# Performance work log

Hardware: AMD Instinct MI355X
Metric: run time of the kernel (lower is better)

Reference implementation:

```python
import jax, jax.numpy as jnp
import numpy as np
import math

HEAD_DIM = 128
N_HEADS = 32
N_KV_HEADS = 8
HIDDEN = 4096
ROPE_BASE = 10000.0


def _rope_cos_sin(position_ids):
    # inv_freq: [D/2]
    inv_freq = 1.0 / (ROPE_BASE ** (jnp.arange(0, HEAD_DIM, 2, dtype=jnp.float32) / HEAD_DIM))
    freqs = position_ids.astype(jnp.float32)[..., None] * inv_freq  # [B,S,D/2]
    emb = jnp.concatenate([freqs, freqs], axis=-1)  # [B,S,D]
    return jnp.cos(emb), jnp.sin(emb)


def _rotate_half(x):
    x1, x2 = jnp.split(x, 2, axis=-1)
    return jnp.concatenate([-x2, x1], axis=-1)


def setup_inputs() -> dict:
    key = jax.random.key(0)
    ks = jax.random.split(key, 5)
    B, S = 1, 2048
    inp = {
        "hidden_states": jax.random.normal(ks[0], (B, S, HIDDEN), dtype=jnp.float32),
        "position_ids": jnp.arange(B * S, dtype=jnp.int32).reshape(B, S),
        "Wq": jax.random.normal(ks[1], (HIDDEN, N_HEADS * HEAD_DIM), dtype=jnp.float32) * 0.02,
        "Wk": jax.random.normal(ks[2], (HIDDEN, N_KV_HEADS * HEAD_DIM), dtype=jnp.float32) * 0.02,
        "Wv": jax.random.normal(ks[3], (HIDDEN, N_KV_HEADS * HEAD_DIM), dtype=jnp.float32) * 0.02,
        "Wo": jax.random.normal(ks[4], (N_HEADS * HEAD_DIM, HIDDEN), dtype=jnp.float32) * 0.02,
    }
    return inp


def reference(hidden_states, position_ids, Wq, Wk, Wv, Wo):
    B, S, _ = hidden_states.shape
    G = N_HEADS // N_KV_HEADS

    q = (hidden_states @ Wq).reshape(B, S, N_HEADS, HEAD_DIM).transpose(0, 2, 1, 3)      # [B,H,S,D]
    k = (hidden_states @ Wk).reshape(B, S, N_KV_HEADS, HEAD_DIM).transpose(0, 2, 1, 3)   # [B,Hkv,S,D]
    v = (hidden_states @ Wv).reshape(B, S, N_KV_HEADS, HEAD_DIM).transpose(0, 2, 1, 3)

    cos, sin = _rope_cos_sin(position_ids)          # [B,S,D]
    cos = cos[:, None, :, :]                         # [B,1,S,D]
    sin = sin[:, None, :, :]
    q = q * cos + _rotate_half(q) * sin
    k = k * cos + _rotate_half(k) * sin

    # GQA head expansion (repeat_interleave over head dim)
    k = jnp.repeat(k, G, axis=1)                     # [B,H,S,D]
    v = jnp.repeat(v, G, axis=1)

    scale = 1.0 / math.sqrt(HEAD_DIM)
    scores = jnp.einsum("bhqd,bhkd->bhqk", q, k) * scale  # [B,H,S,S]
    causal = jnp.triu(jnp.full((S, S), -jnp.inf, dtype=scores.dtype), k=1)
    scores = scores + causal[None, None]
    probs = jax.nn.softmax(scores.astype(jnp.float32), axis=-1).astype(q.dtype)
    ctx = jnp.einsum("bhqk,bhkd->bhqd", probs, v)    # [B,H,S,D]
    ctx = ctx.transpose(0, 2, 1, 3).reshape(B, S, N_HEADS * HEAD_DIM)
    return ctx @ Wo
```

## Files before the change

### kernel.cpp

```cpp
#include <hip/hip_runtime.h>
#include <hip/hip_bf16.h>
#include <math.h>

#define SEQ 2048
#define NHEADS 32
#define NKVH 8
#define HD 128
#define HIDDEN 4096

typedef unsigned short u16;
typedef unsigned int u32;
typedef __attribute__((ext_vector_type(8))) __bf16 bf16x8;
typedef __attribute__((ext_vector_type(4))) float f32x4;
typedef __attribute__((ext_vector_type(4))) u16 u16x4;
typedef __attribute__((ext_vector_type(4))) u32 u32x4;

__device__ __forceinline__ u16 f2bf(float f) {
  u32 u = __builtin_bit_cast(u32, f);
  u32 r = (u + 0x7fffu + ((u >> 16) & 1u)) >> 16;
  return (u16)r;
}
__device__ __forceinline__ float bf2f(u16 h) {
  return __builtin_bit_cast(float, ((u32)h) << 16);
}
__device__ __forceinline__ void gload_lds16(const void* g, void* l) {
  __builtin_amdgcn_global_load_lds(
      (const __attribute__((address_space(1))) u32*)g,
      (__attribute__((address_space(3))) u32*)l, 16, 0, 0);
}

__global__ void __launch_bounds__(256) conv_f2b_vec(const float* __restrict__ in,
                                                    u16* __restrict__ out, const int n) {
  const int i = (blockIdx.x * 256 + threadIdx.x) * 4;
  if (i >= n) return;
  const float4 v = *(const float4*)(in + i);
  u16x4 o;
  o.x = f2bf(v.x); o.y = f2bf(v.y); o.z = f2bf(v.z); o.w = f2bf(v.w);
  *(u16x4*)(out + i) = o;
}

__global__ void __launch_bounds__(256) trans_f2b(const float* __restrict__ in,
                                                 u16* __restrict__ out, const int R, const int C) {
  __shared__ float tile[32][33];
  const int c0 = blockIdx.x * 32, r0 = blockIdx.y * 32;
  const int tx = threadIdx.x & 31, ty = threadIdx.x >> 5;
#pragma unroll
  for (int i = 0; i < 4; ++i)
    tile[ty + i * 8][tx] = in[(size_t)(r0 + ty + i * 8) * C + c0 + tx];
  __syncthreads();
#pragma unroll
  for (int i = 0; i < 4; ++i)
    out[(size_t)(c0 + ty + i * 8) * R + r0 + tx] = f2bf(tile[tx][ty + i * 8]);
}

__global__ void __launch_bounds__(256) trans_b2b(const u16* __restrict__ in,
                                                 u16* __restrict__ out, const int R, const int C) {
  __shared__ u16 tile[32][34];
  const int c0 = blockIdx.x * 32, r0 = blockIdx.y * 32;
  const int tx = threadIdx.x & 31, ty = threadIdx.x >> 5;
#pragma unroll
  for (int i = 0; i < 4; ++i)
    tile[ty + i * 8][tx] = in[(size_t)(r0 + ty + i * 8) * C + c0 + tx];
  __syncthreads();
#pragma unroll
  for (int i = 0; i < 4; ++i)
    out[(size_t)(c0 + ty + i * 8) * R + r0 + tx] = tile[tx][ty + i * 8];
}

__global__ void __launch_bounds__(256) rope_ip(u16* __restrict__ x, const int* __restrict__ pos,
                                               const int lognh, const float oscale) {
  const int idx = blockIdx.x * 256 + threadIdx.x;
  const int j = idx & 63;
  const int hh = (idx >> 6) & ((1 << lognh) - 1);
  const int s = idx >> (6 + lognh);
  if (s >= SEQ) return;
  const float p = (float)pos[s];
  const float invf = __expf((float)j * -0.14391156831212787f);
  const float ang = p * invf;
  const float c = cosf(ang), sn = sinf(ang);
  u16* bp = x + ((size_t)s << (7 + lognh)) + hh * 128 + j;
  const float x1 = bf2f(bp[0]), x2 = bf2f(bp[64]);
  bp[0] = f2bf((x1 * c - x2 * sn) * oscale);
  bp[64] = f2bf((x2 * c + x1 * sn) * oscale);
}

__global__ void __launch_bounds__(256) gemm_bt(
    const u16* __restrict__ A, const u16* __restrict__ B0, const u16* __restrict__ B1,
    const u16* __restrict__ B2, void* __restrict__ C0, void* __restrict__ C1,
    void* __restrict__ C2, const int K, const int n0t, const int n1t,
    const int N0, const int N1, const int N2, const int write_f32) {
  __shared__ u16 As[128 * 64];
  __shared__ u16 Bs[128 * 64];
  const int t = threadIdx.x;
  const int lane = t & 63;
  const int w = t >> 6;
  const int wr = w >> 1, wc = w & 1;

  int bx = blockIdx.x;
  const u16* Bp;
  char* Cw;
  int Nn;
  if (bx < n0t) { Bp = B0; Cw = (char*)C0; Nn = N0; }
  else if (bx < n0t + n1t) { bx -= n0t; Bp = B1; Cw = (char*)C1; Nn = N1; }
  else { bx -= n0t + n1t; Bp = B2; Cw = (char*)C2; Nn = N2; }
  const int row0 = blockIdx.y * 128, col0 = bx * 128;

  f32x4 acc[4][4];
#pragma unroll
  for (int m = 0; m < 4; ++m)
#pragma unroll
    for (int n = 0; n < 4; ++n) acc[m][n] = f32x4{0.f, 0.f, 0.f, 0.f};

  const int nkt = K >> 6;
  for (int kt = 0; kt < nkt; ++kt) {
    const int k0 = kt << 6;
#pragma unroll
    for (int i = 0; i < 4; ++i) {
      const int o = (i * 256 + t) * 16;
      const int row = o >> 7;
      const int slot = (o >> 4) & 7;
      gload_lds16(A + (size_t)(row0 + row) * K + k0 + ((slot ^ (row & 7)) << 3), (char*)As + o);
    }
#pragma unroll
    for (int i = 0; i < 4; ++i) {
      const int o = (i * 256 + t) * 16;
      const int row = o >> 7;
      const int slot = (o >> 4) & 7;
      gload_lds16(Bp + (size_t)(col0 + row) * K + k0 + ((slot ^ (row & 7)) << 3), (char*)Bs + o);
    }
    __syncthreads();
#pragma unroll
    for (int kb = 0; kb < 2; ++kb) {
      bf16x8 af[4], bfr[4];
#pragma unroll
      for (int m = 0; m < 4; ++m) {
        const int row = wr * 64 + m * 16 + (lane & 15);
        const int slot = kb * 4 + (lane >> 4);
        af[m] = *(const bf16x8*)((const char*)As + row * 128 + ((slot ^ (row & 7)) << 4));
      }
#pragma unroll
      for (int n = 0; n < 4; ++n) {
        const int row = wc * 64 + n * 16 + (lane & 15);
        const int slot = kb * 4 + (lane >> 4);
        bfr[n] = *(const bf16x8*)((const char*)Bs + row * 128 + ((slot ^ (row & 7)) << 4));
      }
#pragma unroll
      for (int m = 0; m < 4; ++m)
#pragma unroll
        for (int n = 0; n < 4; ++n)
          acc[m][n] = __builtin_amdgcn_mfma_f32_16x16x32_bf16(af[m], bfr[n], acc[m][n], 0, 0, 0);
    }
    __syncthreads();
  }

  const int rb = row0 + wr * 64 + (lane >> 4) * 4;
  const int cbase = col0 + wc * 64 + (lane & 15);
  if (write_f32) {
    float* C = (float*)Cw;
#pragma unroll
    for (int m = 0; m < 4; ++m)
#pragma unroll
      for (int n = 0; n < 4; ++n)
#pragma unroll
        for (int r = 0; r < 4; ++r)
          C[(size_t)(rb + m * 16 + r) * Nn + cbase + n * 16] = acc[m][n][r];
  } else {
    u16* C = (u16*)Cw;
#pragma unroll
    for (int m = 0; m < 4; ++m)
#pragma unroll
      for (int n = 0; n < 4; ++n)
#pragma unroll
        for (int r = 0; r < 4; ++r)
          C[(size_t)(rb + m * 16 + r) * Nn + cbase + n * 16] = f2bf(acc[m][n][r]);
  }
}

__device__ __forceinline__ void stage_kv(const u16* __restrict__ k, const u16* __restrict__ vt,
                                         const int kvh, const int kv0, u16* KsB, u16* VsB,
                                         const int t) {
#pragma unroll
  for (int i = 0; i < 4; ++i) {
    const int o = (i * 256 + t) * 16;
    const int row = o >> 8;
    const int slot = (o >> 4) & 15;
    gload_lds16(k + (size_t)(kv0 + row) * (NKVH * HD) + kvh * HD + ((slot ^ (row & 7)) << 3),
                (char*)KsB + o);
  }
#pragma unroll
  for (int i = 0; i < 4; ++i) {
    const int o = (i * 256 + t) * 16;
    const int row = o >> 7;
    const int slot = (o >> 4) & 7;
    gload_lds16(vt + (size_t)(kvh * HD + row) * SEQ + kv0 + ((slot ^ (row & 7)) << 3),
                (char*)VsB + o);
  }
}

__global__ void __launch_bounds__(256) attn_fwd(const u16* __restrict__ q, const u16* __restrict__ k,
                                                const u16* __restrict__ vt, u16* __restrict__ ctx) {
  __shared__ u16 Ks[2][64 * 128];
  __shared__ u16 Vs[2][128 * 64];
  const int t = threadIdx.x, lane = t & 63, w = t >> 6;
  const int h = blockIdx.x;
  const int qb = (int)gridDim.y - 1 - (int)blockIdx.y;
  const int kvh = h >> 2;
  const int q0 = qb * 64;
  const int sq_base = q0 + w * 16;
  const int l15 = lane & 15, l4 = lane >> 4;
  const int sq_abs = sq_base + l15;

  bf16x8 qf[4];
  {
    const u16* qp = q + (size_t)sq_abs * (NHEADS * HD) + h * HD + l4 * 8;
#pragma unroll
    for (int kb = 0; kb < 4; ++kb) qf[kb] = *(const bf16x8*)(qp + kb * 32);
  }
  f32x4 po[8];
#pragma unroll
  for (int i = 0; i < 8; ++i) po[i] = f32x4{0.f, 0.f, 0.f, 0.f};
  float mrow = -1e30f;
  float lrow = 0.f;

  const int nb = qb + 1;
  stage_kv(k, vt, kvh, 0, Ks[0], Vs[0], t);
  __syncthreads();
  int cur = 0;

  for (int b = 0; b < nb; ++b) {
    if (b + 1 < nb) stage_kv(k, vt, kvh, (b + 1) * 64, Ks[cur ^ 1], Vs[cur ^ 1], t);

    f32x4 st[4];
#pragma unroll
    for (int c = 0; c < 4; ++c) st[c] = f32x4{0.f, 0.f, 0.f, 0.f};
#pragma unroll
    for (int c = 0; c < 4; ++c) {
      const int row = c * 16 + l15;
#pragma unroll
      for (int kb = 0; kb < 4; ++kb) {
        const int slot = kb * 4 + l4;
        bf16x8 bk = *(const bf16x8*)((const char*)Ks[cur] + row * 256 + ((slot ^ (row & 7)) << 4));
        st[c] = __builtin_amdgcn_mfma_f32_16x16x32_bf16(bk, qf[kb], st[c], 0, 0, 0);
      }
    }

    if (b == nb - 1) {
#pragma unroll
      for (int c = 0; c < 4; ++c)
#pragma unroll
        for (int r = 0; r < 4; ++r) {
          const int sk = b * 64 + c * 16 + l4 * 4 + r;
          if (sk > sq_abs) st[c][r] = -1e30f;
        }
    }

    float rmax = -3e38f;
#pragma unroll
    for (int c = 0; c < 4; ++c)
      rmax = fmaxf(rmax, fmaxf(fmaxf(st[c][0], st[c][1]), fmaxf(st[c][2], st[c][3])));
    rmax = fmaxf(rmax, __shfl_xor(rmax, 16, 64));
    rmax = fmaxf(rmax, __shfl_xor(rmax, 32, 64));

    const bool skip = __all(rmax <= mrow + 8.f);
    const float mnew = skip ? mrow : fmaxf(mrow, rmax);

    float rs = 0.f;
#pragma unroll
    for (int c = 0; c < 4; ++c) {
      const float e0 = exp2f(st[c][0] - mnew), e1 = exp2f(st[c][1] - mnew);
      const float e2 = exp2f(st[c][2] - mnew), e3 = exp2f(st[c][3] - mnew);
      st[c][0] = e0; st[c][1] = e1; st[c][2] = e2; st[c][3] = e3;
      rs += (e0 + e1) + (e2 + e3);
    }
    rs += __shfl_xor(rs, 16, 64);
    rs += __shfl_xor(rs, 32, 64);

    if (!skip) {
      const float alpha = exp2f(mrow - mnew);
      mrow = mnew;
      lrow = lrow * alpha + rs;
      float av[4];
#pragma unroll
      for (int r = 0; r < 4; ++r) av[r] = __shfl(alpha, l4 * 4 + r, 16);
#pragma unroll
      for (int db = 0; db < 8; ++db)
#pragma unroll
        for (int r = 0; r < 4; ++r) po[db][r] *= av[r];
    } else {
      lrow += rs;
    }

    u32 pk[4][2];
#pragma unroll
    for (int c = 0; c < 4; ++c) {
      pk[c][0] = (u32)f2bf(st[c][0]) | ((u32)f2bf(st[c][1]) << 16);
      pk[c][1] = (u32)f2bf(st[c][2]) | ((u32)f2bf(st[c][3]) << 16);
    }
    const int src01 = l15 + ((lane & 16) << 1);
    const int src23 = src01 + 16;
    const bool lo = (lane & 32) == 0;
#pragma unroll
    for (int kb2 = 0; kb2 < 2; ++kb2) {
      const int c0 = kb2 * 2, c1 = c0 + 1;
      const u32 a0 = (u32)__shfl((int)pk[c0][0], src01, 64);
      const u32 a1 = (u32)__shfl((int)pk[c0][1], src01, 64);
      const u32 a2 = (u32)__shfl((int)pk[c0][0], src23, 64);
      const u32 a3 = (u32)__shfl((int)pk[c0][1], src23, 64);
      const u32 b0 = (u32)__shfl((int)pk[c1][0], src01, 64);
      const u32 b1 = (u32)__shfl((int)pk[c1][1], src01, 64);
      const u32 b2 = (u32)__shfl((int)pk[c1][0], src23, 64);
      const u32 b3 = (u32)__shfl((int)pk[c1][1], src23, 64);
      u32x4 wq;
      wq.x = lo ? a0 : b0;
      wq.y = lo ? a1 : b1;
      wq.z = lo ? a2 : b2;
      wq.w = lo ? a3 : b3;
      const bf16x8 pa = __builtin_bit_cast(bf16x8, wq);
#pragma unroll
      for (int db = 0; db < 8; ++db) {
        const int vrow = db * 16 + l15;
        const int pslot = kb2 * 4 + l4;
        bf16x8 bv = *(const bf16x8*)((const char*)Vs[cur] + vrow * 128 + ((pslot ^ (vrow & 7)) << 4));
        po[db] = __builtin_amdgcn_mfma_f32_16x16x32_bf16(pa, bv, po[db], 0, 0, 0);
      }
    }
    __syncthreads();
    cur ^= 1;
  }

  float rl[4];
#pragma unroll
  for (int r = 0; r < 4; ++r) rl[r] = 1.f / __shfl(lrow, l4 * 4 + r, 16);
#pragma unroll
  for (int db = 0; db < 8; ++db)
#pragma unroll
    for (int r = 0; r < 4; ++r) {
      const int sq = sq_base + l4 * 4 + r;
      const int d = db * 16 + l15;
      ctx[(size_t)sq * (NHEADS * HD) + h * HD + d] = f2bf(po[db][r] * rl[r]);
    }
}

extern "C" void kernel_launch(void* const* d_in, const int* in_sizes, int n_in,
                              void* d_out, int out_size, void* d_ws, size_t ws_size,
                              hipStream_t stream) {
  const float* hs = (const float*)d_in[0];
  const int* pos = (const int*)d_in[1];
  const float* Wq = (const float*)d_in[2];
  const float* Wk = (const float*)d_in[3];
  const float* Wv = (const float*)d_in[4];
  const float* Wo = (const float*)d_in[5];

  u16* ws = (u16*)d_ws;
  u16* Xb = ws;
  u16* Wqt = Xb + (size_t)2048 * 4096;
  u16* Wkt = Wqt + (size_t)4096 * 4096;
  u16* Wvt = Wkt + (size_t)1024 * 4096;
  u16* Wot = Wvt + (size_t)1024 * 4096;
  u16* qb = Wot + (size_t)4096 * 4096;
  u16* kb = qb + (size_t)2048 * 4096;
  u16* vb = kb + (size_t)2048 * 1024;
  u16* vtb = vb + (size_t)2048 * 1024;
  u16* ctx = vtb + (size_t)1024 * 2048;
  const size_t need = ((size_t)(ctx - ws) + (size_t)2048 * 4096) * 2;
  if (ws_size < need) return;

  conv_f2b_vec<<<8192, 256, 0, stream>>>(hs, Xb, 2048 * 4096);
  trans_f2b<<<dim3(128, 128), 256, 0, stream>>>(Wq, Wqt, 4096, 4096);
  trans_f2b<<<dim3(32, 128), 256, 0, stream>>>(Wk, Wkt, 4096, 1024);
  trans_f2b<<<dim3(32, 128), 256, 0, stream>>>(Wv, Wvt, 4096, 1024);
  trans_f2b<<<dim3(128, 128), 256, 0, stream>>>(Wo, Wot, 4096, 4096);

  gemm_bt<<<dim3(48, 16), 256, 0, stream>>>(Xb, Wqt, Wkt, Wvt, qb, kb, vb,
                                            4096, 32, 8, 4096, 1024, 1024, 0);

  const float qscale = 0.08838834764831845f * 1.44269504088896340f;
  rope_ip<<<16384, 256, 0, stream>>>(qb, pos, 5, qscale);
  rope_ip<<<4096, 256, 0, stream>>>(kb, pos, 3, 1.0f);

  trans_b2b<<<dim3(32, 64), 256, 0, stream>>>(vb, vtb, 2048, 1024);

  attn_fwd<<<dim3(32, 32), 256, 0, stream>>>(qb, kb, vtb, ctx);

  gemm_bt<<<dim3(32, 16), 256, 0, stream>>>(ctx, Wot, Wot, Wot, d_out, d_out, d_out,
                                            4096, 32, 0, 4096, 4096, 4096, 1);
}
```

Measured before the change: 388.1 us.

## Replace GEMM with 8-wave double-buffered ping-pong kernel and larger tiles

Replaces the simple 128x128 single-buffered GEMM with a 512-thread kernel using 256x256 (QKV) or 128x256 (output) tiles. Shared-memory stages are split into halves and double buffered, so global-to-LDS loads overlap MFMA work. Explicit vmcnt waits and s_setprio raise the priority of the MFMA phases. Block indices are also swizzled for L2 locality. This aims to hide memory latency and improve data reuse, at the cost of more registers and LDS, fewer blocks, and hand-tuned wait counts that must match the number of outstanding loads.

```diff
diff --git a/kernel.cpp b/kernel.cpp
--- a/kernel.cpp
+++ b/kernel.cpp
@@ -84,95 +84,178 @@
   bp[64] = f2bf((x2 * c + x1 * sn) * oscale);
 }
 
-__global__ void __launch_bounds__(256) gemm_bt(
-    const u16* __restrict__ A, const u16* __restrict__ B0, const u16* __restrict__ B1,
-    const u16* __restrict__ B2, void* __restrict__ C0, void* __restrict__ C1,
+template <int MF, int MH, int NH>
+__device__ __forceinline__ void mfmaq(f32x4 (&acc)[MF][4], const bf16x8 (&af)[MF / 2][2],
+                                      const bf16x8 (&bfv)[2][2]) {
+#pragma unroll
+  for (int f = 0; f < MF / 2; ++f)
+#pragma unroll
+    for (int e = 0; e < 2; ++e)
+#pragma unroll
+      for (int ks = 0; ks < 2; ++ks)
+        acc[MH * (MF / 2) + f][NH * 2 + e] = __builtin_amdgcn_mfma_f32_16x16x32_bf16(
+            af[f][ks], bfv[e][ks], acc[MH * (MF / 2) + f][NH * 2 + e], 0, 0, 0);
+}
+
+template <int MF>
+__global__ void __launch_bounds__(512, 2) gemm8p(
+    const u16* __restrict__ A, const u16* __restrict__ B0q, const u16* __restrict__ B1q,
+    const u16* __restrict__ B2q, void* __restrict__ C0, void* __restrict__ C1,
     void* __restrict__ C2, const int K, const int n0t, const int n1t,
     const int N0, const int N1, const int N2, const int write_f32) {
-  __shared__ u16 As[128 * 64];
-  __shared__ u16 Bs[128 * 64];
+  constexpr int BM = MF * 32;
+  constexpr int AHR = BM / 2;
+  constexpr int GA = (AHR * 128) / 8192;
+  __shared__ u16 As[2][2][AHR * 64];
+  __shared__ u16 Bs[2][2][128 * 64];
+
   const int t = threadIdx.x;
   const int lane = t & 63;
   const int w = t >> 6;
-  const int wr = w >> 1, wc = w & 1;
-
-  int bx = blockIdx.x;
-  const u16* Bp;
-  char* Cw;
-  int Nn;
-  if (bx < n0t) { Bp = B0; Cw = (char*)C0; Nn = N0; }
-  else if (bx < n0t + n1t) { bx -= n0t; Bp = B1; Cw = (char*)C1; Nn = N1; }
-  else { bx -= n0t + n1t; Bp = B2; Cw = (char*)C2; Nn = N2; }
-  const int row0 = blockIdx.y * 128, col0 = bx * 128;
-
-  f32x4 acc[4][4];
-#pragma unroll
-  for (int m = 0; m < 4; ++m)
-#pragma unroll
-    for (int n = 0; n < 4; ++n) acc[m][n] = f32x4{0.f, 0.f, 0.f, 0.f};
-
-  const int nkt = K >> 6;
-  for (int kt = 0; kt < nkt; ++kt) {
-    const int k0 = kt << 6;
-#pragma unroll
-    for (int i = 0; i < 4; ++i) {
-      const int o = (i * 256 + t) * 16;
-      const int row = o >> 7;
+  const int wr = w >> 2;
+  const int wc = w & 3;
+  const int l15 = lane & 15, l4 = lane >> 4;
+
+  const int nxt = gridDim.x;
+  int flat = blockIdx.y * nxt + blockIdx.x;
+  flat = (flat & 7) * ((nxt * (int)gridDim.y) >> 3) + (flat >> 3);
+  int bxt = flat % nxt;
+  const int byt = flat / nxt;
+
+  const u16* Bp; char* Cw; int Nn;
+  if (bxt < n0t) { Bp = B0q; Cw = (char*)C0; Nn = N0; }
+  else if (bxt < n0t + n1t) { bxt -= n0t; Bp = B1q; Cw = (char*)C1; Nn = N1; }
+  else { bxt -= n0t + n1t; Bp = B2q; Cw = (char*)C2; Nn = N2; }
+  const int row0 = byt * BM, col0 = bxt * 256;
+
+  auto stageA = [&](int buf, int half, int tile) {
+#pragma unroll
+    for (int g = 0; g < GA; ++g) {
+      const int o = (g * 512 + t) * 16;
+      const int ridx = o >> 7;
       const int slot = (o >> 4) & 7;
-      gload_lds16(A + (size_t)(row0 + row) * K + k0 + ((slot ^ (row & 7)) << 3), (char*)As + o);
-    }
-#pragma unroll
-    for (int i = 0; i < 4; ++i) {
-      const int o = (i * 256 + t) * 16;
-      const int row = o >> 7;
+      const int gr = (ridx / (MF * 8)) * AHR + half * (MF * 8) + (ridx % (MF * 8));
+      gload_lds16(A + (size_t)(row0 + gr) * K + (tile << 6) + ((slot ^ (ridx & 7)) << 3),
+                  (char*)&As[buf][half][0] + o);
+    }
+  };
+  auto stageB = [&](int buf, int half, int tile) {
+#pragma unroll
+    for (int g = 0; g < 2; ++g) {
+      const int o = (g * 512 + t) * 16;
+      const int ridx = o >> 7;
       const int slot = (o >> 4) & 7;
-      gload_lds16(Bp + (size_t)(col0 + row) * K + k0 + ((slot ^ (row & 7)) << 3), (char*)Bs + o);
-    }
-    __syncthreads();
-#pragma unroll
-    for (int kb = 0; kb < 2; ++kb) {
-      bf16x8 af[4], bfr[4];
-#pragma unroll
-      for (int m = 0; m < 4; ++m) {
-        const int row = wr * 64 + m * 16 + (lane & 15);
-        const int slot = kb * 4 + (lane >> 4);
-        af[m] = *(const bf16x8*)((const char*)As + row * 128 + ((slot ^ (row & 7)) << 4));
-      }
-#pragma unroll
-      for (int n = 0; n < 4; ++n) {
-        const int row = wc * 64 + n * 16 + (lane & 15);
-        const int slot = kb * 4 + (lane >> 4);
-        bfr[n] = *(const bf16x8*)((const char*)Bs + row * 128 + ((slot ^ (row & 7)) << 4));
-      }
-#pragma unroll
-      for (int m = 0; m < 4; ++m)
-#pragma unroll
-        for (int n = 0; n < 4; ++n)
-          acc[m][n] = __builtin_amdgcn_mfma_f32_16x16x32_bf16(af[m], bfr[n], acc[m][n], 0, 0, 0);
-    }
-    __syncthreads();
-  }
-
-  const int rb = row0 + wr * 64 + (lane >> 4) * 4;
-  const int cbase = col0 + wc * 64 + (lane & 15);
+      const int gn = (ridx >> 5) * 64 + half * 32 + (ridx & 31);
+      gload_lds16(Bp + (size_t)(col0 + gn) * K + (tile << 6) + ((slot ^ (ridx & 7)) << 3),
+                  (char*)&Bs[buf][half][0] + o);
+    }
+  };
+
+  bf16x8 af[MF / 2][2], bfv[2][2];
+  auto loadA = [&](int buf, int half) {
+#pragma unroll
+    for (int f = 0; f < MF / 2; ++f)
+#pragma unroll
+      for (int ks = 0; ks < 2; ++ks) {
+        const int idx = wr * (MF * 8) + f * 16 + l15;
+        af[f][ks] = *(const bf16x8*)((const char*)&As[buf][half][0] + idx * 128 +
+                                     (((ks * 4 + l4) ^ (idx & 7)) << 4));
+      }
+  };
+  auto loadB = [&](int buf, int half) {
+#pragma unroll
+    for (int e = 0; e < 2; ++e)
+#pragma unroll
+      for (int ks = 0; ks < 2; ++ks) {
+        const int idx = wc * 32 + e * 16 + l15;
+        bfv[e][ks] = *(const bf16x8*)((const char*)&Bs[buf][half][0] + idx * 128 +
+                                      (((ks * 4 + l4) ^ (idx & 7)) << 4));
+      }
+  };
+
+  f32x4 acc[MF][4];
+#pragma unroll
+  for (int m_ = 0; m_ < MF; ++m_)
+#pragma unroll
+    for (int n_ = 0; n_ < 4; ++n_) acc[m_][n_] = f32x4{0.f, 0.f, 0.f, 0.f};
+
+  const int nkt = K >> 6, nit = nkt >> 1;
+
+#define VMW_STEADY                                                  \
+  if constexpr (MF == 8) asm volatile("s_waitcnt vmcnt(4)" ::: "memory"); \
+  else asm volatile("s_waitcnt vmcnt(3)" ::: "memory");
+#define BAR __builtin_amdgcn_s_barrier()
+#define PRIO1 __builtin_amdgcn_s_setprio(1)
+#define PRIO0 __builtin_amdgcn_s_setprio(0)
+
+  stageA(0, 0, 0); stageA(0, 1, 0); stageB(0, 0, 0); stageB(0, 1, 0);
+  stageA(1, 0, 1); stageB(1, 1, 1);
+  VMW_STEADY;
+  BAR;
+
+  for (int i = 0; i < nit; ++i) {
+    const int tb = 2 * i;
+    const bool g2 = (i + 1 < nit);
+    loadA(0, 0); loadB(0, 0);
+    stageA(1, 1, tb + 1);
+    BAR; PRIO1; mfmaq<MF, 0, 0>(acc, af, bfv); PRIO0; BAR;
+    loadB(0, 1);
+    stageB(1, 0, tb + 1);
+    BAR; PRIO1; mfmaq<MF, 0, 1>(acc, af, bfv); PRIO0; BAR;
+    loadA(0, 1);
+    if (g2) stageA(0, 0, tb + 2);
+    BAR; PRIO1; mfmaq<MF, 1, 1>(acc, af, bfv); PRIO0; BAR;
+    loadB(0, 0);
+    if (g2) stageB(0, 1, tb + 2);
+    BAR; PRIO1; mfmaq<MF, 1, 0>(acc, af, bfv); PRIO0;
+    if (g2) { VMW_STEADY; } else { asm volatile("s_waitcnt vmcnt(0)" ::: "memory"); }
+    BAR;
+    loadA(1, 0); loadB(1, 0);
+    if (g2) stageA(0, 1, tb + 2);
+    BAR; PRIO1; mfmaq<MF, 0, 0>(acc, af, bfv); PRIO0; BAR;
+    loadB(1, 1);
+    if (g2) stageB(0, 0, tb + 2);
+    BAR; PRIO1; mfmaq<MF, 0, 1>(acc, af, bfv); PRIO0; BAR;
+    loadA(1, 1);
+    if (g2) stageA(1, 0, tb + 3);
+    BAR; PRIO1; mfmaq<MF, 1, 1>(acc, af, bfv); PRIO0; BAR;
+    loadB(1, 0);
+    if (g2) stageB(1, 1, tb + 3);
+    BAR; PRIO1; mfmaq<MF, 1, 0>(acc, af, bfv); PRIO0;
+    if (g2) { VMW_STEADY; } else { asm volatile("s_waitcnt vmcnt(0)" ::: "memory"); }
+    BAR;
+  }
+#undef VMW_STEADY
+#undef BAR
+#undef PRIO1
+#undef PRIO0
+
   if (write_f32) {
     float* C = (float*)Cw;
 #pragma unroll
-    for (int m = 0; m < 4; ++m)
-#pragma unroll
-      for (int n = 0; n < 4; ++n)
+    for (int am = 0; am < MF; ++am) {
+      const int row = row0 + wr * AHR + (am / (MF / 2)) * (MF * 8) + (am % (MF / 2)) * 16 + l4 * 4;
+#pragma unroll
+      for (int an = 0; an < 4; ++an) {
+        const int col = col0 + wc * 64 + (an >> 1) * 32 + (an & 1) * 16 + l15;
 #pragma unroll
         for (int r = 0; r < 4; ++r)
-          C[(size_t)(rb + m * 16 + r) * Nn + cbase + n * 16] = acc[m][n][r];
+          C[(size_t)(row + r) * Nn + col] = acc[am][an][r];
+      }
+    }
   } else {
     u16* C = (u16*)Cw;
 #pragma unroll
-    for (int m = 0; m < 4; ++m)
-#pragma unroll
-      for (int n = 0; n < 4; ++n)
+    for (int am = 0; am < MF; ++am) {
+      const int row = row0 + wr * AHR + (am / (MF / 2)) * (MF * 8) + (am % (MF / 2)) * 16 + l4 * 4;
+#pragma unroll
+      for (int an = 0; an < 4; ++an) {
+        const int col = col0 + wc * 64 + (an >> 1) * 32 + (an & 1) * 16 + l15;
 #pragma unroll
         for (int r = 0; r < 4; ++r)
-          C[(size_t)(rb + m * 16 + r) * Nn + cbase + n * 16] = f2bf(acc[m][n][r]);
+          C[(size_t)(row + r) * Nn + col] = f2bf(acc[am][an][r]);
+      }
+    }
   }
 }
 
@@ -371,8 +454,8 @@
   trans_f2b<<<dim3(32, 128), 256, 0, stream>>>(Wv, Wvt, 4096, 1024);
   trans_f2b<<<dim3(128, 128), 256, 0, stream>>>(Wo, Wot, 4096, 4096);
 
-  gemm_bt<<<dim3(48, 16), 256, 0, stream>>>(Xb, Wqt, Wkt, Wvt, qb, kb, vb,
-                                            4096, 32, 8, 4096, 1024, 1024, 0);
+  gemm8p<8><<<dim3(24, 8), 512, 0, stream>>>(Xb, Wqt, Wkt, Wvt, qb, kb, vb,
+                                             4096, 16, 4, 4096, 1024, 1024, 0);
 
   const float qscale = 0.08838834764831845f * 1.44269504088896340f;
   rope_ip<<<16384, 256, 0, stream>>>(qb, pos, 5, qscale);
@@ -382,6 +465,6 @@
 
   attn_fwd<<<dim3(32, 32), 256, 0, stream>>>(qb, kb, vtb, ctx);
 
-  gemm_bt<<<dim3(32, 16), 256, 0, stream>>>(ctx, Wot, Wot, Wot, d_out, d_out, d_out,
-                                            4096, 32, 0, 4096, 4096, 4096, 1);
-}
+  gemm8p<4><<<dim3(16, 16), 512, 0, stream>>>(ctx, Wot, Wot, Wot, d_out, d_out, d_out,
+                                              4096, 16, 0, 4096, 4096, 4096, 1);
+}
```

Measured after the change: 375.7 us. 1.03x faster.
